# Performance work log

Measured on AMD Instinct MI355X. Metric: run time of the kernel, lower is better.

## Reference

```python
import jax, jax.numpy as jnp
import numpy as np

NUM_DIM = 1024
NUM_HEAD = 4


def setup_inputs() -> dict:
    key = jax.random.key(0)
    k1, k2, k3, k4, k5, k6 = jax.random.split(key, 6)
    B, N, C = 8, 2048, NUM_DIM
    x = jax.random.normal(k1, (B, N, C), dtype=jnp.float32)
    tmp_token = jax.random.normal(k2, (1, 1, C), dtype=jnp.float32)
    s = 1.0 / np.sqrt(C)
    Wqkv = jax.random.uniform(k3, (C, 3 * C), dtype=jnp.float32, minval=-s, maxval=s)
    bqkv = jax.random.uniform(k4, (3 * C,), dtype=jnp.float32, minval=-s, maxval=s)
    # Note: original module zero-inits v_proj; we use random weights for a
    # non-degenerate correctness baseline.
    Wv = jax.random.uniform(k5, (C, C), dtype=jnp.float32, minval=-s, maxval=s)
    bv = jax.random.uniform(k6, (C,), dtype=jnp.float32, minval=-s, maxval=s)
    return {"input": x, "tmp_token": tmp_token, "Wqkv": Wqkv, "bqkv": bqkv, "Wv": Wv, "bv": bv}


def reference(input, tmp_token, Wqkv, bqkv, Wv, bv):
    B = input.shape[0]
    # prepend learned token -> [B, N+1, C]
    x = jnp.concatenate([jnp.broadcast_to(tmp_token, (B, 1, tmp_token.shape[-1])), input], axis=1)
    B, N, C = x.shape
    H, Dh = NUM_HEAD, C // NUM_HEAD
    qkv = (x @ Wqkv + bqkv).reshape(B, N, 3, H, Dh)
    q = qkv[:, :, 0].transpose(0, 2, 1, 3)  # [B, H, N, Dh]
    k = qkv[:, :, 1].transpose(0, 2, 1, 3)
    v = qkv[:, :, 2].transpose(0, 2, 1, 3)
    scale = Dh ** (-0.5)
    scores = jnp.einsum("bhqd,bhkd->bhqk", q, k) * scale
    att = jax.nn.softmax(scores, axis=-1)  # dropout is identity in eval mode
    out = jnp.einsum("bhqk,bhkd->bhqd", att, v)
    out = out.transpose(0, 2, 1, 3).reshape(B, N, C)
    out = out @ Wv + bv  # op dropout identity in eval
    return out[:, 0, :]
```

## Files before the change

### kernel.cpp

```cpp
#include <hip/hip_runtime.h>
#include <math.h>

#define CDIM 1024
#define TC   3072
#define BATCH 8
#define NTOK 2049
#define NIN  2048
#define NHEAD 4

#define OFF_Q0 0
#define OFF_OC 1024
#define ZERO_FLOATS 9216
#define OFF_CK 9216
#define OFF_WS 9728
#define OFF_SC 13824
#define OFF_YP 79392

__global__ void k_q0(const float* __restrict__ t, const float* __restrict__ W,
                     float* __restrict__ wsb) {
    int ic = blockIdx.x >> 3, jc = blockIdx.x & 7;
    int j = jc * 128 + threadIdx.x;
    int i0 = ic * 128;
    float acc = 0.f;
    for (int i = 0; i < 128; ++i)
        acc += t[i0 + i] * W[(size_t)(i0 + i) * TC + j];
    atomicAdd(&wsb[OFF_Q0 + j], acc);
}

__global__ void k_ws(const float* __restrict__ W, const float* __restrict__ bqkv,
                     float* __restrict__ wsb) {
    int wave = threadIdx.x >> 6, lane = threadIdx.x & 63;
    int gw = blockIdx.x * 4 + wave;
    int c = gw >> 2, h = gw & 3;
    int d0 = h * 256 + lane * 4;
    float4 wv = *(const float4*)&W[(size_t)c * TC + CDIM + d0];
    float q0 = wsb[OFF_Q0 + d0]     + bqkv[d0];
    float q1 = wsb[OFF_Q0 + d0 + 1] + bqkv[d0 + 1];
    float q2 = wsb[OFF_Q0 + d0 + 2] + bqkv[d0 + 2];
    float q3 = wsb[OFF_Q0 + d0 + 3] + bqkv[d0 + 3];
    float acc = wv.x * q0 + wv.y * q1 + wv.z * q2 + wv.w * q3;
    float ck = 0.f;
    bool doCk = (blockIdx.x == 0);
    if (doCk) {
        float4 bk = *(const float4*)&bqkv[CDIM + d0];
        ck = bk.x * q0 + bk.y * q1 + bk.z * q2 + bk.w * q3;
    }
    for (int off = 32; off > 0; off >>= 1) {
        acc += __shfl_down(acc, off);
        ck  += __shfl_down(ck, off);
    }
    if (lane == 0) {
        wsb[OFF_WS + h * CDIM + c] = acc;
        if (doCk) wsb[OFF_CK + h] = ck;
    }
}

__global__ __launch_bounds__(1024) void k_scores(const float* __restrict__ x,
                                                 const float* __restrict__ t,
                                                 float* __restrict__ wsb) {
    __shared__ float WsL[4 * CDIM];
    __shared__ float ckL[4];
    for (int i = threadIdx.x; i < 4 * CDIM; i += 1024) WsL[i] = wsb[OFF_WS + i];
    if (threadIdx.x < 4) ckL[threadIdx.x] = wsb[OFF_CK + threadIdx.x];
    __syncthreads();
    int w = threadIdx.x >> 6, lane = threadIdx.x & 63;
    int r = blockIdx.x * 16 + w;
    if (r >= BATCH * NTOK) return;
    int b = r / NTOK, n = r % NTOK;
    const float* row = (n == 0) ? t : x + ((size_t)b * NIN + (n - 1)) * CDIM;
    float a0 = 0.f, a1 = 0.f, a2 = 0.f, a3 = 0.f;
#pragma unroll
    for (int k = 0; k < 4; ++k) {
        int c0 = k * 256 + lane * 4;
        float4 xv = *(const float4*)(row + c0);
        float4 w0 = *(const float4*)&WsL[0 * CDIM + c0];
        float4 w1 = *(const float4*)&WsL[1 * CDIM + c0];
        float4 w2 = *(const float4*)&WsL[2 * CDIM + c0];
        float4 w3 = *(const float4*)&WsL[3 * CDIM + c0];
        a0 += xv.x * w0.x + xv.y * w0.y + xv.z * w0.z + xv.w * w0.w;
        a1 += xv.x * w1.x + xv.y * w1.y + xv.z * w1.z + xv.w * w1.w;
        a2 += xv.x * w2.x + xv.y * w2.y + xv.z * w2.z + xv.w * w2.w;
        a3 += xv.x * w3.x + xv.y * w3.y + xv.z * w3.z + xv.w * w3.w;
    }
    for (int off = 32; off > 0; off >>= 1) {
        a0 += __shfl_down(a0, off);
        a1 += __shfl_down(a1, off);
        a2 += __shfl_down(a2, off);
        a3 += __shfl_down(a3, off);
    }
    if (lane == 0) {
        const float scale = 0.0625f;
        wsb[OFF_SC + ((size_t)b * 4 + 0) * NTOK + n] = (a0 + ckL[0]) * scale;
        wsb[OFF_SC + ((size_t)b * 4 + 1) * NTOK + n] = (a1 + ckL[1]) * scale;
        wsb[OFF_SC + ((size_t)b * 4 + 2) * NTOK + n] = (a2 + ckL[2]) * scale;
        wsb[OFF_SC + ((size_t)b * 4 + 3) * NTOK + n] = (a3 + ckL[3]) * scale;
    }
}

__global__ void k_softmax(float* __restrict__ wsb) {
    float* sc = wsb + OFF_SC + (size_t)blockIdx.x * NTOK;
    __shared__ float redM[4];
    __shared__ float redS[4];
    int tid = threadIdx.x, lane = tid & 63, w = tid >> 6;
    float m = -1e30f;
    for (int n = tid; n < NTOK; n += 256) m = fmaxf(m, sc[n]);
    for (int off = 32; off > 0; off >>= 1) m = fmaxf(m, __shfl_down(m, off));
    if (lane == 0) redM[w] = m;
    __syncthreads();
    m = fmaxf(fmaxf(redM[0], redM[1]), fmaxf(redM[2], redM[3]));
    float s = 0.f;
    for (int n = tid; n < NTOK; n += 256) s += expf(sc[n] - m);
    for (int off = 32; off > 0; off >>= 1) s += __shfl_down(s, off);
    if (lane == 0) redS[w] = s;
    __syncthreads();
    s = redS[0] + redS[1] + redS[2] + redS[3];
    float inv = 1.f / s;
    for (int n = tid; n < NTOK; n += 256) sc[n] = expf(sc[n] - m) * inv;
}

__global__ void k_y(const float* __restrict__ x, const float* __restrict__ t,
                    float* __restrict__ wsb) {
    int b = blockIdx.x >> 5, ch = blockIdx.x & 31;
    int n0 = ch * 65;
    int nend = min(n0 + 65, NTOK);
    int cnt = nend - n0;
    __shared__ float attL[4][65];
    for (int idx = threadIdx.x; idx < 4 * 65; idx += 256) {
        int h = idx / 65, i = idx % 65;
        attL[h][i] = (i < cnt) ? wsb[OFF_SC + ((size_t)b * 4 + h) * NTOK + n0 + i] : 0.f;
    }
    __syncthreads();
    int c0 = threadIdx.x * 4;
    float4 acc[4];
#pragma unroll
    for (int h = 0; h < 4; ++h) acc[h] = make_float4(0.f, 0.f, 0.f, 0.f);
    for (int i = 0; i < cnt; ++i) {
        int n = n0 + i;
        const float* row = (n == 0) ? t : x + ((size_t)b * NIN + (n - 1)) * CDIM;
        float4 xv = *(const float4*)(row + c0);
#pragma unroll
        for (int h = 0; h < 4; ++h) {
            float a = attL[h][i];
            acc[h].x += a * xv.x; acc[h].y += a * xv.y;
            acc[h].z += a * xv.z; acc[h].w += a * xv.w;
        }
    }
#pragma unroll
    for (int h = 0; h < 4; ++h)
        *(float4*)&wsb[OFF_YP + ((size_t)(b * 32 + ch) * 4 + h) * CDIM + c0] = acc[h];
}

__global__ void k_ocy(const float* __restrict__ W, const float* __restrict__ bqkv,
                      float* __restrict__ wsb) {
    int p = blockIdx.x >> 3, q = blockIdx.x & 7;
    int h = p >> 1;
    __shared__ float sL[1024];
    for (int bb = 0; bb < 8; ++bb) {
        float sum = 0.f;
        for (int chn = 0; chn < 32; ++chn)
            sum += wsb[OFF_YP + ((size_t)(bb * 32 + chn) * 4 + h) * CDIM + q * 128 + threadIdx.x];
        sL[bb * 128 + threadIdx.x] = sum;
    }
    __syncthreads();
    int cp = p * 128 + threadIdx.x;
    float acc[8] = {0.f, 0.f, 0.f, 0.f, 0.f, 0.f, 0.f, 0.f};
    for (int c = 0; c < 128; ++c) {
        float wv = W[(size_t)(q * 128 + c) * TC + 2 * CDIM + cp];
#pragma unroll
        for (int bb = 0; bb < 8; ++bb) acc[bb] += sL[bb * 128 + c] * wv;
    }
    if (q == 0) {
        float bias = bqkv[2 * CDIM + cp];
#pragma unroll
        for (int bb = 0; bb < 8; ++bb) acc[bb] += bias;
    }
#pragma unroll
    for (int bb = 0; bb < 8; ++bb) atomicAdd(&wsb[OFF_OC + bb * CDIM + cp], acc[bb]);
}

__global__ void k_out(const float* __restrict__ Wv, const float* __restrict__ bv,
                      const float* __restrict__ wsb, float* __restrict__ out) {
    int jp = blockIdx.x >> 3, cq = blockIdx.x & 7;
    __shared__ float ocL[1024];
    for (int bb = 0; bb < 8; ++bb)
        ocL[bb * 128 + threadIdx.x] = wsb[OFF_OC + bb * CDIM + cq * 128 + threadIdx.x];
    __syncthreads();
    int j = jp * 128 + threadIdx.x;
    float acc[8] = {0.f, 0.f, 0.f, 0.f, 0.f, 0.f, 0.f, 0.f};
    for (int c = 0; c < 128; ++c) {
        float wv = Wv[(size_t)(cq * 128 + c) * CDIM + j];
#pragma unroll
        for (int bb = 0; bb < 8; ++bb) acc[bb] += ocL[bb * 128 + c] * wv;
    }
    if (cq == 0) {
        float bias = bv[j];
#pragma unroll
        for (int bb = 0; bb < 8; ++bb) acc[bb] += bias;
    }
#pragma unroll
    for (int bb = 0; bb < 8; ++bb) atomicAdd(&out[bb * CDIM + j], acc[bb]);
}

extern "C" void kernel_launch(void* const* d_in, const int* in_sizes, int n_in,
                              void* d_out, int out_size, void* d_ws, size_t ws_size,
                              hipStream_t stream) {
    const float* x    = (const float*)d_in[0];
    const float* t    = (const float*)d_in[1];
    const float* Wqkv = (const float*)d_in[2];
    const float* bqkv = (const float*)d_in[3];
    const float* Wv   = (const float*)d_in[4];
    const float* bv   = (const float*)d_in[5];
    float* wsb = (float*)d_ws;
    float* out = (float*)d_out;

    hipMemsetAsync(wsb, 0, ZERO_FLOATS * sizeof(float), stream);
    hipMemsetAsync(out, 0, (size_t)out_size * sizeof(float), stream);

    k_q0     <<<64,   128, 0, stream>>>(t, Wqkv, wsb);
    k_ws     <<<1024, 256, 0, stream>>>(Wqkv, bqkv, wsb);
    k_scores <<<1025, 1024, 0, stream>>>(x, t, wsb);
    k_softmax<<<32,   256, 0, stream>>>(wsb);
    k_y      <<<256,  256, 0, stream>>>(x, t, wsb);
    k_ocy    <<<64,   128, 0, stream>>>(Wqkv, bqkv, wsb);
    k_out    <<<64,   128, 0, stream>>>(Wv, bv, wsb, out);
}
```

Baseline: 187.7 us.

## Fuse scores, softmax and weighted sum into single-pass online-softmax kernel

Replaces the separate scores, softmax and weighted-sum kernels with a single pass over x that computes per-head scores and keeps an online-softmax running max, sum and weighted accumulator per wave. Per-block partials are then merged in a small combine kernel that also folds in the prepended token. The aim is to read x once instead of twice and drop the score round-trips, at the cost of more registers and extra partial-result traffic. It also widens the parallelism of the q0 kernel and drops the constant key-bias term, which cancels in softmax.

```diff
diff --git a/kernel.cpp b/kernel.cpp
--- a/kernel.cpp
+++ b/kernel.cpp
@@ -4,25 +4,25 @@
 #define CDIM 1024
 #define TC   3072
 #define BATCH 8
-#define NTOK 2049
-#define NIN  2048
+#define NIN   2048
 #define NHEAD 4
 
 #define OFF_Q0 0
 #define OFF_OC 1024
 #define ZERO_FLOATS 9216
-#define OFF_CK 9216
-#define OFF_WS 9728
-#define OFF_SC 13824
-#define OFF_YP 79392
+#define OFF_WS 9216
+#define OFF_PM 13312
+#define OFF_PS 15360
+#define OFF_PY 17408
+#define OFF_YB 2114560
 
 __global__ void k_q0(const float* __restrict__ t, const float* __restrict__ W,
                      float* __restrict__ wsb) {
     int ic = blockIdx.x >> 3, jc = blockIdx.x & 7;
     int j = jc * 128 + threadIdx.x;
-    int i0 = ic * 128;
+    int i0 = ic * 32;
     float acc = 0.f;
-    for (int i = 0; i < 128; ++i)
+    for (int i = 0; i < 32; ++i)
         acc += t[i0 + i] * W[(size_t)(i0 + i) * TC + j];
     atomicAdd(&wsb[OFF_Q0 + j], acc);
 }
@@ -39,115 +39,146 @@
     float q2 = wsb[OFF_Q0 + d0 + 2] + bqkv[d0 + 2];
     float q3 = wsb[OFF_Q0 + d0 + 3] + bqkv[d0 + 3];
     float acc = wv.x * q0 + wv.y * q1 + wv.z * q2 + wv.w * q3;
-    float ck = 0.f;
-    bool doCk = (blockIdx.x == 0);
-    if (doCk) {
-        float4 bk = *(const float4*)&bqkv[CDIM + d0];
-        ck = bk.x * q0 + bk.y * q1 + bk.z * q2 + bk.w * q3;
-    }
-    for (int off = 32; off > 0; off >>= 1) {
-        acc += __shfl_down(acc, off);
-        ck  += __shfl_down(ck, off);
-    }
-    if (lane == 0) {
-        wsb[OFF_WS + h * CDIM + c] = acc;
-        if (doCk) wsb[OFF_CK + h] = ck;
-    }
-}
-
-__global__ __launch_bounds__(1024) void k_scores(const float* __restrict__ x,
-                                                 const float* __restrict__ t,
-                                                 float* __restrict__ wsb) {
-    __shared__ float WsL[4 * CDIM];
-    __shared__ float ckL[4];
-    for (int i = threadIdx.x; i < 4 * CDIM; i += 1024) WsL[i] = wsb[OFF_WS + i];
-    if (threadIdx.x < 4) ckL[threadIdx.x] = wsb[OFF_CK + threadIdx.x];
-    __syncthreads();
-    int w = threadIdx.x >> 6, lane = threadIdx.x & 63;
-    int r = blockIdx.x * 16 + w;
-    if (r >= BATCH * NTOK) return;
-    int b = r / NTOK, n = r % NTOK;
-    const float* row = (n == 0) ? t : x + ((size_t)b * NIN + (n - 1)) * CDIM;
-    float a0 = 0.f, a1 = 0.f, a2 = 0.f, a3 = 0.f;
-#pragma unroll
-    for (int k = 0; k < 4; ++k) {
-        int c0 = k * 256 + lane * 4;
-        float4 xv = *(const float4*)(row + c0);
-        float4 w0 = *(const float4*)&WsL[0 * CDIM + c0];
-        float4 w1 = *(const float4*)&WsL[1 * CDIM + c0];
-        float4 w2 = *(const float4*)&WsL[2 * CDIM + c0];
-        float4 w3 = *(const float4*)&WsL[3 * CDIM + c0];
-        a0 += xv.x * w0.x + xv.y * w0.y + xv.z * w0.z + xv.w * w0.w;
-        a1 += xv.x * w1.x + xv.y * w1.y + xv.z * w1.z + xv.w * w1.w;
-        a2 += xv.x * w2.x + xv.y * w2.y + xv.z * w2.z + xv.w * w2.w;
-        a3 += xv.x * w3.x + xv.y * w3.y + xv.z * w3.z + xv.w * w3.w;
-    }
-    for (int off = 32; off > 0; off >>= 1) {
-        a0 += __shfl_down(a0, off);
-        a1 += __shfl_down(a1, off);
-        a2 += __shfl_down(a2, off);
-        a3 += __shfl_down(a3, off);
-    }
-    if (lane == 0) {
-        const float scale = 0.0625f;
-        wsb[OFF_SC + ((size_t)b * 4 + 0) * NTOK + n] = (a0 + ckL[0]) * scale;
-        wsb[OFF_SC + ((size_t)b * 4 + 1) * NTOK + n] = (a1 + ckL[1]) * scale;
-        wsb[OFF_SC + ((size_t)b * 4 + 2) * NTOK + n] = (a2 + ckL[2]) * scale;
-        wsb[OFF_SC + ((size_t)b * 4 + 3) * NTOK + n] = (a3 + ckL[3]) * scale;
-    }
-}
-
-__global__ void k_softmax(float* __restrict__ wsb) {
-    float* sc = wsb + OFF_SC + (size_t)blockIdx.x * NTOK;
-    __shared__ float redM[4];
-    __shared__ float redS[4];
-    int tid = threadIdx.x, lane = tid & 63, w = tid >> 6;
-    float m = -1e30f;
-    for (int n = tid; n < NTOK; n += 256) m = fmaxf(m, sc[n]);
-    for (int off = 32; off > 0; off >>= 1) m = fmaxf(m, __shfl_down(m, off));
-    if (lane == 0) redM[w] = m;
-    __syncthreads();
-    m = fmaxf(fmaxf(redM[0], redM[1]), fmaxf(redM[2], redM[3]));
-    float s = 0.f;
-    for (int n = tid; n < NTOK; n += 256) s += expf(sc[n] - m);
-    for (int off = 32; off > 0; off >>= 1) s += __shfl_down(s, off);
-    if (lane == 0) redS[w] = s;
-    __syncthreads();
-    s = redS[0] + redS[1] + redS[2] + redS[3];
-    float inv = 1.f / s;
-    for (int n = tid; n < NTOK; n += 256) sc[n] = expf(sc[n] - m) * inv;
-}
-
-__global__ void k_y(const float* __restrict__ x, const float* __restrict__ t,
-                    float* __restrict__ wsb) {
-    int b = blockIdx.x >> 5, ch = blockIdx.x & 31;
-    int n0 = ch * 65;
-    int nend = min(n0 + 65, NTOK);
-    int cnt = nend - n0;
-    __shared__ float attL[4][65];
-    for (int idx = threadIdx.x; idx < 4 * 65; idx += 256) {
-        int h = idx / 65, i = idx % 65;
-        attL[h][i] = (i < cnt) ? wsb[OFF_SC + ((size_t)b * 4 + h) * NTOK + n0 + i] : 0.f;
-    }
-    __syncthreads();
-    int c0 = threadIdx.x * 4;
-    float4 acc[4];
-#pragma unroll
-    for (int h = 0; h < 4; ++h) acc[h] = make_float4(0.f, 0.f, 0.f, 0.f);
-    for (int i = 0; i < cnt; ++i) {
-        int n = n0 + i;
-        const float* row = (n == 0) ? t : x + ((size_t)b * NIN + (n - 1)) * CDIM;
-        float4 xv = *(const float4*)(row + c0);
+    for (int off = 32; off > 0; off >>= 1) acc += __shfl_down(acc, off);
+    if (lane == 0) wsb[OFF_WS + h * CDIM + c] = acc;
+}
+
+__global__ __launch_bounds__(256) void k_pass1(const float* __restrict__ x,
+                                               float* __restrict__ wsb) {
+    int tid = threadIdx.x, lane = tid & 63, wave = tid >> 6;
+    int b = blockIdx.x >> 6, blkc = blockIdx.x & 63;
+
+    float4 wsr[4][4];
+#pragma unroll
+    for (int k = 0; k < 4; ++k)
+#pragma unroll
+        for (int h = 0; h < 4; ++h)
+            wsr[k][h] = *(const float4*)&wsb[OFF_WS + h * CDIM + k * 256 + lane * 4];
+
+    float m[4], s[4];
+    float4 y[4][4];
+#pragma unroll
+    for (int h = 0; h < 4; ++h) {
+        m[h] = -1e30f; s[h] = 0.f;
+#pragma unroll
+        for (int k = 0; k < 4; ++k) y[h][k] = make_float4(0.f, 0.f, 0.f, 0.f);
+    }
+
+    const float* base = x + ((size_t)b * NIN + blkc * 32 + wave * 8) * CDIM;
+#pragma unroll 2
+    for (int i = 0; i < 8; ++i) {
+        const float* row = base + (size_t)i * CDIM;
+        float4 xv[4];
+#pragma unroll
+        for (int k = 0; k < 4; ++k) xv[k] = *(const float4*)&row[k * 256 + lane * 4];
+        float d[4];
 #pragma unroll
         for (int h = 0; h < 4; ++h) {
-            float a = attL[h][i];
-            acc[h].x += a * xv.x; acc[h].y += a * xv.y;
-            acc[h].z += a * xv.z; acc[h].w += a * xv.w;
+            float a = 0.f;
+#pragma unroll
+            for (int k = 0; k < 4; ++k)
+                a += xv[k].x * wsr[k][h].x + xv[k].y * wsr[k][h].y +
+                     xv[k].z * wsr[k][h].z + xv[k].w * wsr[k][h].w;
+            for (int off = 1; off < 64; off <<= 1) a += __shfl_xor(a, off);
+            d[h] = a * 0.0625f;
         }
-    }
-#pragma unroll
-    for (int h = 0; h < 4; ++h)
-        *(float4*)&wsb[OFF_YP + ((size_t)(b * 32 + ch) * 4 + h) * CDIM + c0] = acc[h];
+#pragma unroll
+        for (int h = 0; h < 4; ++h) {
+            float sc = d[h], f;
+            if (sc > m[h]) {
+                float rs = __expf(m[h] - sc);
+                s[h] *= rs;
+#pragma unroll
+                for (int k = 0; k < 4; ++k) {
+                    y[h][k].x *= rs; y[h][k].y *= rs; y[h][k].z *= rs; y[h][k].w *= rs;
+                }
+                m[h] = sc; f = 1.f;
+            } else f = __expf(sc - m[h]);
+            s[h] += f;
+#pragma unroll
+            for (int k = 0; k < 4; ++k) {
+                y[h][k].x += f * xv[k].x; y[h][k].y += f * xv[k].y;
+                y[h][k].z += f * xv[k].z; y[h][k].w += f * xv[k].w;
+            }
+        }
+    }
+
+    __shared__ float ms[4][4], ss[4][4];
+    __shared__ float ybuf[4][CDIM];
+    if (lane == 0)
+#pragma unroll
+        for (int h = 0; h < 4; ++h) { ms[wave][h] = m[h]; ss[wave][h] = s[h]; }
+    for (int idx = tid; idx < 4 * CDIM; idx += 256) ((float*)ybuf)[idx] = 0.f;
+    __syncthreads();
+    float mb[4], sb[4], fme[4];
+#pragma unroll
+    for (int h = 0; h < 4; ++h) {
+        mb[h] = fmaxf(fmaxf(ms[0][h], ms[1][h]), fmaxf(ms[2][h], ms[3][h]));
+        sb[h] = 0.f;
+#pragma unroll
+        for (int w = 0; w < 4; ++w) sb[h] += __expf(ms[w][h] - mb[h]) * ss[w][h];
+        fme[h] = __expf(m[h] - mb[h]);
+    }
+    for (int w = 0; w < 4; ++w) {
+        if (wave == w) {
+#pragma unroll
+            for (int h = 0; h < 4; ++h)
+#pragma unroll
+                for (int k = 0; k < 4; ++k) {
+                    float4* dst = (float4*)&ybuf[h][k * 256 + lane * 4];
+                    float4 v = *dst;
+                    v.x += fme[h] * y[h][k].x; v.y += fme[h] * y[h][k].y;
+                    v.z += fme[h] * y[h][k].z; v.w += fme[h] * y[h][k].w;
+                    *dst = v;
+                }
+        }
+        __syncthreads();
+    }
+    int p = blockIdx.x;
+    if (tid < 4) { wsb[OFF_PM + p * 4 + tid] = mb[tid]; wsb[OFF_PS + p * 4 + tid] = sb[tid]; }
+    for (int idx = tid; idx < 4 * CDIM; idx += 256)
+        wsb[OFF_PY + (size_t)p * 4096 + idx] = ((float*)ybuf)[idx];
+}
+
+__global__ void k_comb(const float* __restrict__ t, float* __restrict__ wsb) {
+    int tid = threadIdx.x, lane = tid & 63, wv = tid >> 6;
+    int blk = blockIdx.x;
+    int b = blk >> 4, h = (blk >> 2) & 3, cq = blk & 3;
+    __shared__ float red[4], redM[4], redS[4], fbuf[64];
+
+    int c0 = tid * 4;
+    float4 tv = *(const float4*)&t[c0];
+    float4 wsv = *(const float4*)&wsb[OFF_WS + h * CDIM + c0];
+    float p = tv.x * wsv.x + tv.y * wsv.y + tv.z * wsv.z + tv.w * wsv.w;
+    for (int off = 1; off < 64; off <<= 1) p += __shfl_xor(p, off);
+    if (lane == 0) red[wv] = p;
+    __syncthreads();
+    float sc0 = (red[0] + red[1] + red[2] + red[3]) * 0.0625f;
+
+    float mv = (tid < 64) ? wsb[OFF_PM + (size_t)(b * 64 + tid) * 4 + h] : -1e30f;
+    float mr = mv;
+    for (int off = 1; off < 64; off <<= 1) mr = fmaxf(mr, __shfl_xor(mr, off));
+    if (lane == 0) redM[wv] = mr;
+    __syncthreads();
+    float M = fmaxf(fmaxf(fmaxf(redM[0], redM[1]), fmaxf(redM[2], redM[3])), sc0);
+
+    float sv = 0.f;
+    if (tid < 64) {
+        float fj = __expf(mv - M);
+        fbuf[tid] = fj;
+        sv = fj * wsb[OFF_PS + (size_t)(b * 64 + tid) * 4 + h];
+    }
+    for (int off = 1; off < 64; off <<= 1) sv += __shfl_xor(sv, off);
+    if (lane == 0) redS[wv] = sv;
+    __syncthreads();
+    float e0 = __expf(sc0 - M);
+    float S = redS[0] + redS[1] + redS[2] + redS[3] + e0;
+
+    int c = cq * 256 + tid;
+    float acc = e0 * t[c];
+    for (int j = 0; j < 64; ++j)
+        acc += fbuf[j] * wsb[OFF_PY + (size_t)(b * 64 + j) * 4096 + h * CDIM + c];
+    wsb[OFF_YB + (size_t)(b * 4 + h) * CDIM + c] = acc / S;
 }
 
 __global__ void k_ocy(const float* __restrict__ W, const float* __restrict__ bqkv,
@@ -155,12 +186,8 @@
     int p = blockIdx.x >> 3, q = blockIdx.x & 7;
     int h = p >> 1;
     __shared__ float sL[1024];
-    for (int bb = 0; bb < 8; ++bb) {
-        float sum = 0.f;
-        for (int chn = 0; chn < 32; ++chn)
-            sum += wsb[OFF_YP + ((size_t)(bb * 32 + chn) * 4 + h) * CDIM + q * 128 + threadIdx.x];
-        sL[bb * 128 + threadIdx.x] = sum;
-    }
+    for (int bb = 0; bb < 8; ++bb)
+        sL[bb * 128 + threadIdx.x] = wsb[OFF_YB + (size_t)(bb * 4 + h) * CDIM + q * 128 + threadIdx.x];
     __syncthreads();
     int cp = p * 128 + threadIdx.x;
     float acc[8] = {0.f, 0.f, 0.f, 0.f, 0.f, 0.f, 0.f, 0.f};
@@ -216,11 +243,10 @@
     hipMemsetAsync(wsb, 0, ZERO_FLOATS * sizeof(float), stream);
     hipMemsetAsync(out, 0, (size_t)out_size * sizeof(float), stream);
 
-    k_q0     <<<64,   128, 0, stream>>>(t, Wqkv, wsb);
-    k_ws     <<<1024, 256, 0, stream>>>(Wqkv, bqkv, wsb);
-    k_scores <<<1025, 1024, 0, stream>>>(x, t, wsb);
-    k_softmax<<<32,   256, 0, stream>>>(wsb);
-    k_y      <<<256,  256, 0, stream>>>(x, t, wsb);
-    k_ocy    <<<64,   128, 0, stream>>>(Wqkv, bqkv, wsb);
-    k_out    <<<64,   128, 0, stream>>>(Wv, bv, wsb, out);
-}
+    k_q0   <<<256,  128, 0, stream>>>(t, Wqkv, wsb);
+    k_ws   <<<1024, 256, 0, stream>>>(Wqkv, bqkv, wsb);
+    k_pass1<<<512,  256, 0, stream>>>(x, wsb);
+    k_comb <<<128,  256, 0, stream>>>(t, wsb);
+    k_ocy  <<<64,   128, 0, stream>>>(Wqkv, bqkv, wsb);
+    k_out  <<<64,   128, 0, stream>>>(Wv, bv, wsb, out);
+}
```

Result: faster. 182.2 us (-2.9%).
